# Optimization experiments

Measured on AMD Instinct MI355X. Metric: run time of the kernel, lower is better.

The kernel has to match this reference:

```python
import jax, jax.numpy as jnp
import numpy as np

B, H, S, D = 4, 16, 2048, 64
NEG = -1e9  # matches torch masked_fill(-1000000000.0)

def setup_inputs() -> dict:
    key = jax.random.key(0)
    kq, kk, kv, km = jax.random.split(key, 4)
    q = jax.random.normal(kq, (B, H, S, D), dtype=jnp.float32)
    k = jax.random.normal(kk, (B, H, S, D), dtype=jnp.float32)
    v = jax.random.normal(kv, (B, H, S, D), dtype=jnp.float32)
    key_padding_mask = jax.random.bernoulli(km, 0.1, (B, S))
    return {"q": q, "k": k, "v": v, "key_padding_mask": key_padding_mask}

def reference(q, k, v, key_padding_mask):
    d_k = q.shape[-1]
    scale = 1.0 / jnp.sqrt(jnp.asarray(d_k, dtype=q.dtype))
    # [B,H,S,S]
    scores = jnp.einsum('bhqd,bhkd->bhqk', q, k) * scale
    scores = jnp.where(key_padding_mask[:, None, None, :], NEG, scores)
    attn = jax.nn.softmax(scores, axis=-1)  # dropout p=0.0 -> identity
    return jnp.einsum('bhqk,bhkd->bhqd', attn, v)
```

## Files before the change

### kernel.cpp

```cpp
#include <hip/hip_runtime.h>
#include <hip/hip_bf16.h>

#define SQ 2048
#define DD 64
#define NBH 64
#define KVB 64
#define NT (SQ / KVB)
#define REC 16384
#define VOFF 8192
#define SCL 0.18033688011112042f

typedef __attribute__((ext_vector_type(8))) short bf16x8;
typedef __attribute__((ext_vector_type(4))) float f32x4;
typedef __attribute__((ext_vector_type(16))) float f32x16;

__device__ __forceinline__ short f2bf(float f) {
  union { float f; unsigned u; } un; un.f = f;
  unsigned r = un.u + 0x7fffu + ((un.u >> 16) & 1u);
  return (short)(r >> 16);
}

__device__ __forceinline__ unsigned cvtpk(float lo, float hi) {
  unsigned d;
  asm("v_cvt_pk_bf16_f32 %0, %1, %2" : "=v"(d) : "v"(lo), "v"(hi));
  return d;
}

__device__ __forceinline__ void gld_lds16(const void* g, void* l) {
  __builtin_amdgcn_global_load_lds(
      (const __attribute__((address_space(1))) unsigned int*)g,
      (__attribute__((address_space(3))) unsigned int*)l, 16, 0, 0);
}

__device__ __forceinline__ f32x16 z16() {
  f32x16 z;
  #pragma unroll
  for (int i = 0; i < 16; ++i) z[i] = 0.f;
  return z;
}


__global__ __launch_bounds__(256)
void prepack(const float* __restrict__ Kg, const float* __restrict__ Vg,
             const int* __restrict__ maskg, char* __restrict__ img)
{
  __shared__ float vst[64][68];
  const int bh = blockIdx.y, t = blockIdx.x;
  const size_t base = ((size_t)bh * SQ + (size_t)t * KVB) * DD;
  const int r  = threadIdx.x >> 2;
  const int q4 = threadIdx.x & 3;
  const int c0 = q4 * 16;
  char* rec = img + ((size_t)bh * NT + t) * REC;
  const int* mrow = maskg + (size_t)(bh >> 4) * SQ + t * KVB;
  unsigned long long mb = __ballot(mrow[threadIdx.x & 63] != 0);

  {
    const float* g = Vg + base + (size_t)r * DD + c0;
    #pragma unroll
    for (int i = 0; i < 4; ++i)
      *(f32x4*)&vst[r][c0 + i * 4] = *(const f32x4*)&g[i * 4];
  }
  {
    const float* g = Kg + base + (size_t)r * DD + c0;
    float tv[16];
    #pragma unroll
    for (int i = 0; i < 4; ++i) *(f32x4*)&tv[i * 4] = *(const f32x4*)&g[i * 4];
    bf16x8 lo, hi8;
    #pragma unroll
    for (int j = 0; j < 8; ++j) { lo[j] = f2bf(tv[j]); hi8[j] = f2bf(tv[8 + j]); }
    char* p = rec + r * 128;
    *(bf16x8*)(p + (((2 * q4)     ^ (r & 7)) << 4)) = lo;
    *(bf16x8*)(p + (((2 * q4 + 1) ^ (r & 7)) << 4)) = hi8;
  }
  __syncthreads();
  {
    const int d = r;
    bf16x8 lo, hi8;
    #pragma unroll
    for (int j = 0; j < 8; ++j) {
      int k0 = 8 * q4 + (j & 3) + 32 * ((j >> 2) & 1);
      int k1 = k0 + 4;
      lo[j]  = ((mb >> k0) & 1ull) ? (short)0 : f2bf(vst[k0][d]);
      hi8[j] = ((mb >> k1) & 1ull) ? (short)0 : f2bf(vst[k1][d]);
    }
    char* p = rec + VOFF + d * 128;
    *(bf16x8*)(p + (((2 * q4)     ^ (d & 7)) << 4)) = lo;
    *(bf16x8*)(p + (((2 * q4 + 1) ^ (d & 7)) << 4)) = hi8;
  }
}

__global__ __launch_bounds__(256)
void attn32(const char* __restrict__ img, const float* __restrict__ Qg,
            const int* __restrict__ maskg, float* __restrict__ Og)
{
  __shared__ char buf[2][REC];
  __shared__ __align__(16) short mones[NT][KVB];

  const int tid  = threadIdx.x;
  const int wv   = tid >> 6;
  const int lane = tid & 63;
  const int l31  = lane & 31;
  const int hi   = lane >> 5;

  const int bid = blockIdx.x;
  const int swz = (bid & 7) * 128 + (bid >> 3);
  const int qb = swz & 15;
  const int bh = swz >> 4;
  const int q0 = qb * 128 + wv * 32;
  const size_t base = (size_t)bh * SQ * DD;
  const char* rec0 = img + (size_t)bh * NT * REC;

  {
    const int* mrow = maskg + (size_t)(bh >> 4) * SQ;
    #pragma unroll
    for (int i = 0; i < 8; ++i) {
      int idx = tid + i * 256;
      int t = idx >> 6, p = idx & 63;
      int kv = 8 * (p >> 4) + 4 * ((p >> 3) & 1) + (p & 3) + 32 * ((p >> 2) & 1);
      mones[t][p] = mrow[t * KVB + kv] ? (short)0 : (short)0x3F80;
    }
  }

  int slotoff[4];
  #pragma unroll
  for (int kk = 0; kk < 4; ++kk)
    slotoff[kk] = (((2 * kk + hi) ^ (l31 & 7)) << 4);
  const int rbase = l31 * 128;

  bf16x8 qf[4];
  {
    const float* qrow = Qg + base + (size_t)(q0 + l31) * DD + hi * 8;
    #pragma unroll
    for (int kk = 0; kk < 4; ++kk) {
      float tv[8];
      *(f32x4*)&tv[0] = *(const f32x4*)&qrow[kk * 16];
      *(f32x4*)&tv[4] = *(const f32x4*)&qrow[kk * 16 + 4];
      #pragma unroll
      for (int j = 0; j < 8; ++j) qf[kk][j] = f2bf(tv[j] * SCL);
    }
  }

  #pragma unroll
  for (int i = 0; i < 4; ++i)
    gld_lds16(rec0 + i * 4096 + tid * 16, buf[0] + i * 4096 + tid * 16);

  f32x16 accO0 = z16(), accO1 = z16(), acc2 = z16();

  int cur = 0;
  for (int t = 0; t < NT; ++t) {
    __syncthreads();

    if (t + 1 < NT) {
      const char* rec = rec0 + (size_t)(t + 1) * REC;
      char* dst = buf[cur ^ 1];
      #pragma unroll
      for (int i = 0; i < 4; ++i)
        gld_lds16(rec + i * 4096 + tid * 16, dst + i * 4096 + tid * 16);
    }

    const char* bk = buf[cur];
    f32x16 sA = z16(), sB = z16();
    #pragma unroll
    for (int kk = 0; kk < 4; ++kk) {
      bf16x8 k0 = *(const bf16x8*)(bk + rbase + slotoff[kk]);
      bf16x8 k1 = *(const bf16x8*)(bk + 4096 + rbase + slotoff[kk]);
      sA = __builtin_amdgcn_mfma_f32_32x32x16_bf16(k0, qf[kk], sA, 0, 0, 0);
      sB = __builtin_amdgcn_mfma_f32_32x32x16_bf16(k1, qf[kk], sB, 0, 0, 0);
    }

    #pragma unroll
    for (int r = 0; r < 16; ++r) {
      sA[r] = exp2f(sA[r]);
      sB[r] = exp2f(sB[r]);
    }

    const short* mrowt = &mones[t][0];
    #pragma unroll
    for (int kk = 0; kk < 4; ++kk) {
      union { unsigned u[4]; bf16x8 v; } pf;
      pf.u[0] = cvtpk(sA[4 * kk + 0], sA[4 * kk + 1]);
      pf.u[1] = cvtpk(sA[4 * kk + 2], sA[4 * kk + 3]);
      pf.u[2] = cvtpk(sB[4 * kk + 0], sB[4 * kk + 1]);
      pf.u[3] = cvtpk(sB[4 * kk + 2], sB[4 * kk + 3]);
      bf16x8 vf0 = *(const bf16x8*)(bk + VOFF + rbase + slotoff[kk]);
      bf16x8 vf1 = *(const bf16x8*)(bk + VOFF + 4096 + rbase + slotoff[kk]);
      bf16x8 of  = *(const bf16x8*)(mrowt + (2 * kk + hi) * 8);
      accO0 = __builtin_amdgcn_mfma_f32_32x32x16_bf16(pf.v, vf0, accO0, 0, 0, 0);
      accO1 = __builtin_amdgcn_mfma_f32_32x32x16_bf16(pf.v, vf1, accO1, 0, 0, 0);
      acc2  = __builtin_amdgcn_mfma_f32_32x32x16_bf16(pf.v, of,  acc2,  0, 0, 0);
    }
    cur ^= 1;
  }

  #pragma unroll
  for (int reg = 0; reg < 16; ++reg) {
    int ql = (reg & 3) + 8 * (reg >> 2) + 4 * hi;
    float iq = 1.0f / acc2[reg];
    float* orow = Og + base + (size_t)(q0 + ql) * DD;
    orow[l31]      = accO0[reg] * iq;
    orow[32 + l31] = accO1[reg] * iq;
  }
}

__global__ __launch_bounds__(256)
void attn_fallback(const float* __restrict__ Qg, const float* __restrict__ Kg,
                   const float* __restrict__ Vg, const int* __restrict__ maskg,
                   float* __restrict__ Og)
{
  __shared__ short ktf[KVB][72];
  __shared__ short vtf[DD][72];
  __shared__ short ptf[4][16][72];
  __shared__ float bias_s[KVB];

  const int tid = threadIdx.x, wv = tid >> 6, lane = tid & 63;
  const int l15 = lane & 15, lg = lane >> 4;
  const int bh = blockIdx.y, bb = bh >> 4, q0 = blockIdx.x * 64;
  const size_t base = (size_t)bh * SQ * DD;
  const f32x4 zero4 = {0.f, 0.f, 0.f, 0.f};

  bf16x8 qf[2];
  {
    const float* qrow = Qg + base + (size_t)(q0 + wv * 16 + l15) * DD + lg * 8;
    #pragma unroll
    for (int kf = 0; kf < 2; ++kf) {
      float tv[8];
      *(f32x4*)&tv[0] = *(const f32x4*)&qrow[kf * 32];
      *(f32x4*)&tv[4] = *(const f32x4*)&qrow[kf * 32 + 4];
      #pragma unroll
      for (int j = 0; j < 8; ++j) qf[kf][j] = f2bf(tv[j]);
    }
  }
  f32x4 oacc[4];
  #pragma unroll
  for (int d = 0; d < 4; ++d) oacc[d] = zero4;
  float mrun[4] = {-3e38f, -3e38f, -3e38f, -3e38f};
  float lrun[4] = {0.f, 0.f, 0.f, 0.f};

  for (int kv0 = 0; kv0 < SQ; kv0 += KVB) {
    __syncthreads();
    {
      int r = tid >> 2, c0 = (tid & 3) * 16;
      const float* g = Kg + base + (size_t)(kv0 + r) * DD + c0;
      float tv[16];
      #pragma unroll
      for (int i = 0; i < 4; ++i) *(f32x4*)&tv[i * 4] = *(const f32x4*)&g[i * 4];
      bf16x8 a, b2;
      #pragma unroll
      for (int j = 0; j < 8; ++j) { a[j] = f2bf(tv[j]); b2[j] = f2bf(tv[8 + j]); }
      *(bf16x8*)&ktf[r][c0] = a;
      *(bf16x8*)&ktf[r][c0 + 8] = b2;
    }
    {
      int r = tid & 63, c0 = (tid >> 6) * 16;
      const float* g = Vg + base + (size_t)(kv0 + r) * DD + c0;
      float tv[16];
      #pragma unroll
      for (int i = 0; i < 4; ++i) *(f32x4*)&tv[i * 4] = *(const f32x4*)&g[i * 4];
      #pragma unroll
      for (int j = 0; j < 16; ++j) vtf[c0 + j][r] = f2bf(tv[j]);
    }
    if (tid < KVB) bias_s[tid] = maskg[(size_t)bb * SQ + kv0 + tid] ? -1e9f : 0.f;
    __syncthreads();

    f32x4 acc[4];
    #pragma unroll
    for (int n = 0; n < 4; ++n) acc[n] = zero4;
    #pragma unroll
    for (int n = 0; n < 4; ++n) {
      bf16x8 k0 = *(const bf16x8*)&ktf[n * 16 + l15][lg * 8];
      bf16x8 k1 = *(const bf16x8*)&ktf[n * 16 + l15][32 + lg * 8];
      acc[n] = __builtin_amdgcn_mfma_f32_16x16x32_bf16(qf[0], k0, acc[n], 0, 0, 0);
      acc[n] = __builtin_amdgcn_mfma_f32_16x16x32_bf16(qf[1], k1, acc[n], 0, 0, 0);
    }
    float brow[4];
    #pragma unroll
    for (int n = 0; n < 4; ++n) brow[n] = bias_s[n * 16 + l15];
    #pragma unroll
    for (int reg = 0; reg < 4; ++reg) {
      float s0 = acc[0][reg] * 0.125f + brow[0];
      float s1 = acc[1][reg] * 0.125f + brow[1];
      float s2 = acc[2][reg] * 0.125f + brow[2];
      float s3 = acc[3][reg] * 0.125f + brow[3];
      float tm = fmaxf(fmaxf(s0, s1), fmaxf(s2, s3));
      #pragma unroll
      for (int off = 1; off < 16; off <<= 1) tm = fmaxf(tm, __shfl_xor(tm, off, 64));
      float mnew = fmaxf(mrun[reg], tm);
      float scale = __expf(mrun[reg] - mnew);
      float p0 = __expf(s0 - mnew), p1 = __expf(s1 - mnew);
      float p2 = __expf(s2 - mnew), p3 = __expf(s3 - mnew);
      float rs = (p0 + p1) + (p2 + p3);
      #pragma unroll
      for (int off = 1; off < 16; off <<= 1) rs += __shfl_xor(rs, off, 64);
      lrun[reg] = lrun[reg] * scale + rs;
      mrun[reg] = mnew;
      #pragma unroll
      for (int d = 0; d < 4; ++d) oacc[d][reg] *= scale;
      int prow = lg * 4 + reg;
      ptf[wv][prow][     l15] = f2bf(p0);
      ptf[wv][prow][16 + l15] = f2bf(p1);
      ptf[wv][prow][32 + l15] = f2bf(p2);
      ptf[wv][prow][48 + l15] = f2bf(p3);
    }
    bf16x8 pf0 = *(const bf16x8*)&ptf[wv][l15][lg * 8];
    bf16x8 pf1 = *(const bf16x8*)&ptf[wv][l15][32 + lg * 8];
    #pragma unroll
    for (int d = 0; d < 4; ++d) {
      bf16x8 v0 = *(const bf16x8*)&vtf[d * 16 + l15][lg * 8];
      bf16x8 v1 = *(const bf16x8*)&vtf[d * 16 + l15][32 + lg * 8];
      oacc[d] = __builtin_amdgcn_mfma_f32_16x16x32_bf16(pf0, v0, oacc[d], 0, 0, 0);
      oacc[d] = __builtin_amdgcn_mfma_f32_16x16x32_bf16(pf1, v1, oacc[d], 0, 0, 0);
    }
  }
  #pragma unroll
  for (int reg = 0; reg < 4; ++reg) {
    float inv = 1.0f / lrun[reg];
    int row = q0 + wv * 16 + lg * 4 + reg;
    float* orow = Og + base + (size_t)row * DD;
    #pragma unroll
    for (int d = 0; d < 4; ++d) orow[d * 16 + l15] = oacc[d][reg] * inv;
  }
}

extern "C" void kernel_launch(void* const* d_in, const int* in_sizes, int n_in,
                              void* d_out, int out_size, void* d_ws, size_t ws_size,
                              hipStream_t stream) {
  const float* q    = (const float*)d_in[0];
  const float* k    = (const float*)d_in[1];
  const float* v    = (const float*)d_in[2];
  const int*   mask = (const int*)d_in[3];
  float* out = (float*)d_out;

  const size_t need = (size_t)NBH * NT * REC;
  if (ws_size >= need) {
    char* img = (char*)d_ws;
    dim3 pgrid(NT, NBH);
    prepack<<<pgrid, 256, 0, stream>>>(k, v, mask, img);
    attn32<<<dim3(1024), 256, 0, stream>>>(img, q, mask, out);
  } else {
    dim3 grid(SQ / 64, NBH);
    attn_fallback<<<grid, 256, 0, stream>>>(q, k, v, mask, out);
  }
}
```

Measured before the change: 143.5 us.

## Prepack K/V in MFMA fragment order and read directly from global memory

The prepack kernel now writes K and V tiles in per-lane MFMA fragment order, so each lane's 16-byte operand sits contiguously at lane*16 within 1 KB chunks. The attention kernel drops its LDS double buffer, its global_load_lds prefetch and the per-tile barrier, and loads MFMA operands straight from global memory (served from L2/cache). This removes LDS traffic and synchronisation and frees LDS for occupancy. The cost is that global load latency is exposed on each tile with no explicit software prefetch.

```diff
diff --git a/kernel.cpp b/kernel.cpp
--- a/kernel.cpp
+++ b/kernel.cpp
@@ -26,12 +26,6 @@
   return d;
 }
 
-__device__ __forceinline__ void gld_lds16(const void* g, void* l) {
-  __builtin_amdgcn_global_load_lds(
-      (const __attribute__((address_space(1))) unsigned int*)g,
-      (__attribute__((address_space(3))) unsigned int*)l, 16, 0, 0);
-}
-
 __device__ __forceinline__ f32x16 z16() {
   f32x16 z;
   #pragma unroll
@@ -47,45 +41,50 @@
   __shared__ float vst[64][68];
   const int bh = blockIdx.y, t = blockIdx.x;
   const size_t base = ((size_t)bh * SQ + (size_t)t * KVB) * DD;
-  const int r  = threadIdx.x >> 2;
-  const int q4 = threadIdx.x & 3;
-  const int c0 = q4 * 16;
+  const int tid  = threadIdx.x;
+  const int wv   = tid >> 6;
+  const int lane = tid & 63;
+  const int l31  = lane & 31;
+  const int hi   = lane >> 5;
   char* rec = img + ((size_t)bh * NT + t) * REC;
   const int* mrow = maskg + (size_t)(bh >> 4) * SQ + t * KVB;
-  unsigned long long mb = __ballot(mrow[threadIdx.x & 63] != 0);
+  unsigned long long mb = __ballot(mrow[lane] != 0);
 
   {
+    int r = tid >> 2, c0 = (tid & 3) * 16;
     const float* g = Vg + base + (size_t)r * DD + c0;
     #pragma unroll
     for (int i = 0; i < 4; ++i)
       *(f32x4*)&vst[r][c0 + i * 4] = *(const f32x4*)&g[i * 4];
   }
-  {
-    const float* g = Kg + base + (size_t)r * DD + c0;
-    float tv[16];
-    #pragma unroll
-    for (int i = 0; i < 4; ++i) *(f32x4*)&tv[i * 4] = *(const f32x4*)&g[i * 4];
-    bf16x8 lo, hi8;
-    #pragma unroll
-    for (int j = 0; j < 8; ++j) { lo[j] = f2bf(tv[j]); hi8[j] = f2bf(tv[8 + j]); }
-    char* p = rec + r * 128;
-    *(bf16x8*)(p + (((2 * q4)     ^ (r & 7)) << 4)) = lo;
-    *(bf16x8*)(p + (((2 * q4 + 1) ^ (r & 7)) << 4)) = hi8;
+  #pragma unroll
+  for (int i = 0; i < 2; ++i) {
+    int cid = wv * 2 + i;
+    int kk = cid >> 1, h = cid & 1;
+    int r = h * 32 + l31;
+    int c = (2 * kk + hi) * 8;
+    const float* g = Kg + base + (size_t)r * DD + c;
+    float tv[8];
+    *(f32x4*)&tv[0] = *(const f32x4*)&g[0];
+    *(f32x4*)&tv[4] = *(const f32x4*)&g[4];
+    bf16x8 o;
+    #pragma unroll
+    for (int j = 0; j < 8; ++j) o[j] = f2bf(tv[j]);
+    *(bf16x8*)(rec + cid * 1024 + lane * 16) = o;
   }
   __syncthreads();
-  {
-    const int d = r;
-    bf16x8 lo, hi8;
+  #pragma unroll
+  for (int i = 0; i < 2; ++i) {
+    int cid = wv * 2 + i;
+    int kk = cid >> 1, h = cid & 1;
+    int d = h * 32 + l31;
+    bf16x8 o;
     #pragma unroll
     for (int j = 0; j < 8; ++j) {
-      int k0 = 8 * q4 + (j & 3) + 32 * ((j >> 2) & 1);
-      int k1 = k0 + 4;
-      lo[j]  = ((mb >> k0) & 1ull) ? (short)0 : f2bf(vst[k0][d]);
-      hi8[j] = ((mb >> k1) & 1ull) ? (short)0 : f2bf(vst[k1][d]);
-    }
-    char* p = rec + VOFF + d * 128;
-    *(bf16x8*)(p + (((2 * q4)     ^ (d & 7)) << 4)) = lo;
-    *(bf16x8*)(p + (((2 * q4 + 1) ^ (d & 7)) << 4)) = hi8;
+      int kv = 8 * kk + 4 * hi + (j & 3) + 32 * (j >> 2);
+      o[j] = ((mb >> kv) & 1ull) ? (short)0 : f2bf(vst[kv][d]);
+    }
+    *(bf16x8*)(rec + VOFF + cid * 1024 + lane * 16) = o;
   }
 }
 
@@ -93,7 +92,6 @@
 void attn32(const char* __restrict__ img, const float* __restrict__ Qg,
             const int* __restrict__ maskg, float* __restrict__ Og)
 {
-  __shared__ char buf[2][REC];
   __shared__ __align__(16) short mones[NT][KVB];
 
   const int tid  = threadIdx.x;
@@ -121,12 +119,6 @@
     }
   }
 
-  int slotoff[4];
-  #pragma unroll
-  for (int kk = 0; kk < 4; ++kk)
-    slotoff[kk] = (((2 * kk + hi) ^ (l31 & 7)) << 4);
-  const int rbase = l31 * 128;
-
   bf16x8 qf[4];
   {
     const float* qrow = Qg + base + (size_t)(q0 + l31) * DD + hi * 8;
@@ -140,30 +132,19 @@
     }
   }
 
-  #pragma unroll
-  for (int i = 0; i < 4; ++i)
-    gld_lds16(rec0 + i * 4096 + tid * 16, buf[0] + i * 4096 + tid * 16);
-
+  __syncthreads();
+
+  const int loff = lane * 16;
   f32x16 accO0 = z16(), accO1 = z16(), acc2 = z16();
 
-  int cur = 0;
   for (int t = 0; t < NT; ++t) {
-    __syncthreads();
-
-    if (t + 1 < NT) {
-      const char* rec = rec0 + (size_t)(t + 1) * REC;
-      char* dst = buf[cur ^ 1];
-      #pragma unroll
-      for (int i = 0; i < 4; ++i)
-        gld_lds16(rec + i * 4096 + tid * 16, dst + i * 4096 + tid * 16);
-    }
-
-    const char* bk = buf[cur];
+    const char* rec = rec0 + (size_t)t * REC;
+
     f32x16 sA = z16(), sB = z16();
     #pragma unroll
     for (int kk = 0; kk < 4; ++kk) {
-      bf16x8 k0 = *(const bf16x8*)(bk + rbase + slotoff[kk]);
-      bf16x8 k1 = *(const bf16x8*)(bk + 4096 + rbase + slotoff[kk]);
+      bf16x8 k0 = *(const bf16x8*)(rec + (kk * 2 + 0) * 1024 + loff);
+      bf16x8 k1 = *(const bf16x8*)(rec + (kk * 2 + 1) * 1024 + loff);
       sA = __builtin_amdgcn_mfma_f32_32x32x16_bf16(k0, qf[kk], sA, 0, 0, 0);
       sB = __builtin_amdgcn_mfma_f32_32x32x16_bf16(k1, qf[kk], sB, 0, 0, 0);
     }
@@ -182,14 +163,13 @@
       pf.u[1] = cvtpk(sA[4 * kk + 2], sA[4 * kk + 3]);
       pf.u[2] = cvtpk(sB[4 * kk + 0], sB[4 * kk + 1]);
       pf.u[3] = cvtpk(sB[4 * kk + 2], sB[4 * kk + 3]);
-      bf16x8 vf0 = *(const bf16x8*)(bk + VOFF + rbase + slotoff[kk]);
-      bf16x8 vf1 = *(const bf16x8*)(bk + VOFF + 4096 + rbase + slotoff[kk]);
+      bf16x8 vf0 = *(const bf16x8*)(rec + VOFF + (kk * 2 + 0) * 1024 + loff);
+      bf16x8 vf1 = *(const bf16x8*)(rec + VOFF + (kk * 2 + 1) * 1024 + loff);
       bf16x8 of  = *(const bf16x8*)(mrowt + (2 * kk + hi) * 8);
       accO0 = __builtin_amdgcn_mfma_f32_32x32x16_bf16(pf.v, vf0, accO0, 0, 0, 0);
       accO1 = __builtin_amdgcn_mfma_f32_32x32x16_bf16(pf.v, vf1, accO1, 0, 0, 0);
       acc2  = __builtin_amdgcn_mfma_f32_32x32x16_bf16(pf.v, of,  acc2,  0, 0, 0);
     }
-    cur ^= 1;
   }
 
   #pragma unroll
```

New measurement: 205.6 us. 1.43x slower.
